# Optimization experiments

Hardware: AMD Instinct MI355X
Metric: run time of the kernel (lower is better)

Reference implementation:

```python
import jax, jax.numpy as jnp
import numpy as np

B, T, F, H = 64, 2048, 128, 32  # batch, seq_len, input_features, lstm hidden


def setup_inputs() -> dict:
    key = jax.random.key(0)
    ks = jax.random.split(key, 4)
    X = jax.random.normal(ks[0], (B, T, F), dtype=jnp.float32)
    # combined gate weights, order (i, f, g, o) as in flax.linen.LSTMCell
    Wx = jax.random.normal(ks[1], (F, 4 * H), dtype=jnp.float32) / np.float32(np.sqrt(F))
    Wh = jax.random.normal(ks[2], (H, 4 * H), dtype=jnp.float32) / np.float32(np.sqrt(H))
    b = jnp.zeros((4 * H,), dtype=jnp.float32)
    Wd = jax.random.normal(ks[3], (H, 1), dtype=jnp.float32) / np.float32(np.sqrt(H))
    bd = jnp.zeros((1,), dtype=jnp.float32)
    return {"X": X, "Wx": Wx, "Wh": Wh, "b": b, "Wd": Wd, "bd": bd}


def reference(X, Wx, Wh, b, Wd, bd):
    # Precompute input->gate projections for all timesteps in one GEMM.
    xg = jnp.einsum('btf,fg->btg', X, Wx) + b  # [B, T, 4H]

    def step(carry, xg_t):
        c, h = carry
        g = xg_t + h @ Wh  # [B, 4H]
        i, f, gc, o = jnp.split(g, 4, axis=-1)
        c = jax.nn.sigmoid(f) * c + jax.nn.sigmoid(i) * jnp.tanh(gc)
        h = jax.nn.sigmoid(o) * jnp.tanh(c)
        return (c, h), None

    zeros = jnp.zeros((X.shape[0], H), X.dtype)
    (c_T, h_T), _ = jax.lax.scan(step, (zeros, zeros), jnp.swapaxes(xg, 0, 1))
    # Dense(1) applied to outputs, then last timestep selected == Dense on h_T
    return h_T @ Wd + bd  # [B, 1]
```

## Files before the change

kernel.cpp:

```cpp
#include <hip/hip_runtime.h>
#include <math.h>

#define BB 64
#define TT 2048
#define FF 128
#define HH 32
#define GG 128

#define S1f (-1.4426950408889634f)
#define S2f (-2.8853900817779268f)

typedef _Float16 half2_t __attribute__((ext_vector_type(2)));

__device__ __forceinline__ unsigned h2u(half2_t v) {
    unsigned u; __builtin_memcpy(&u, &v, 4); return u;
}
__device__ __forceinline__ half2_t u2h(unsigned u) {
    half2_t v; __builtin_memcpy(&v, &u, 4); return v;
}
__device__ __forceinline__ half2_t pkrtz(float a, float b) {
    auto r = __builtin_amdgcn_cvt_pkrtz(a, b);
    half2_t v; __builtin_memcpy(&v, &r, 4); return v;
}
__device__ __forceinline__ float rcp_(float x) { return __builtin_amdgcn_rcpf(x); }
__device__ __forceinline__ float exp2_(float x) { return __builtin_amdgcn_exp2f(x); }

#define DPP_(x, ctrl) \
    ((unsigned)__builtin_amdgcn_mov_dpp((int)(x), (ctrl), 0xF, 0xF, true))
#define CTRL_XOR1 0xB1
#define CTRL_XOR2 0x4E
#define CTRL_ROR4 0x124
#define CTRL_ROR8 0x128
#define SWZ16_(x) ((unsigned)__builtin_amdgcn_ds_swizzle((int)(x), 0x401F))

__global__ __launch_bounds__(256) void xg_gemm(const float* __restrict__ X,
                                               const float* __restrict__ Wx,
                                               const float* __restrict__ bias,
                                               float* __restrict__ xgT) {
    __shared__ float XL[64 * 32];
    __shared__ float WL[32 * 128];
    const int tid = threadIdx.x;
    const int row0 = blockIdx.x * 64;
    const int j0 = (tid & 15) * 8;
    const int r0 = (tid >> 4) * 4;

    float acc[4][8];
#pragma unroll
    for (int r = 0; r < 4; ++r)
#pragma unroll
        for (int jj = 0; jj < 8; ++jj) acc[r][jj] = 0.f;

    for (int f0 = 0; f0 < FF; f0 += 32) {
        __syncthreads();
        {
            const float4* src = (const float4*)(Wx + f0 * GG);
            float4* dst = (float4*)WL;
            dst[tid]       = src[tid];
            dst[tid + 256] = src[tid + 256];
            dst[tid + 512] = src[tid + 512];
            dst[tid + 768] = src[tid + 768];
        }
        {
            int lin = tid * 4;
            int row = lin >> 5;
            int fi  = lin & 31;
            ((float4*)XL)[tid] =
                *(const float4*)(X + (size_t)(row0 + row) * FF + f0 + fi);
            lin = (tid + 256) * 4;
            row = lin >> 5;
            fi  = lin & 31;
            ((float4*)XL)[tid + 256] =
                *(const float4*)(X + (size_t)(row0 + row) * FF + f0 + fi);
        }
        __syncthreads();
#pragma unroll 4
        for (int fi = 0; fi < 32; ++fi) {
            float xv[4];
#pragma unroll
            for (int r = 0; r < 4; ++r) xv[r] = XL[(r0 + r) * 32 + fi];
            float4 w0 = *(float4*)&WL[fi * GG + j0];
            float4 w1 = *(float4*)&WL[fi * GG + j0 + 4];
            float w[8] = {w0.x, w0.y, w0.z, w0.w, w1.x, w1.y, w1.z, w1.w};
#pragma unroll
            for (int r = 0; r < 4; ++r)
#pragma unroll
                for (int jj = 0; jj < 8; ++jj)
                    acc[r][jj] = fmaf(xv[r], w[jj], acc[r][jj]);
        }
    }
    const int b  = row0 >> 11;
    const int t0 = (row0 & 2047) + r0;
    float bl[8];
#pragma unroll
    for (int jj = 0; jj < 8; ++jj) bl[jj] = bias[j0 + jj];
#pragma unroll
    for (int jj = 0; jj < 8; ++jj) {
        const int j = j0 + jj;
        const float sc = (j >= 64 && j < 96) ? S2f : S1f;
        float4 o;
        o.x = (acc[0][jj] + bl[jj]) * sc;
        o.y = (acc[1][jj] + bl[jj]) * sc;
        o.z = (acc[2][jj] + bl[jj]) * sc;
        o.w = (acc[3][jj] + bl[jj]) * sc;
        *(float4*)(xgT + ((size_t)b * GG + j) * TT + t0) = o;
    }
}

__global__ __launch_bounds__(64) void lstm_rec(const float* __restrict__ xgT,
                                               const float* __restrict__ Wh,
                                               const float* __restrict__ Wd,
                                               const float* __restrict__ bd,
                                               float* __restrict__ out) {
    const int l = threadIdx.x;
    const int m = l & 31;
    const bool lo = (l < HH);
    const int b = blockIdx.x;

    unsigned iv[16];
    iv[0] = (unsigned)m;
    iv[1] = SWZ16_(iv[0]);
    iv[2] = DPP_(iv[0], CTRL_XOR2);
    iv[3] = DPP_(iv[1], CTRL_XOR2);
#pragma unroll
    for (int r = 0; r < 4; ++r) iv[4 + r] = DPP_(iv[r], CTRL_ROR4);
#pragma unroll
    for (int r = 0; r < 8; ++r) iv[8 + r] = DPP_(iv[r], CTRL_ROR8);

    const float scx = S1f;
    const float scy = lo ? S2f : S1f;
    half2_t whx[16], why[16];
#pragma unroll
    for (int r = 0; r < 16; ++r) {
        const int p  = (int)(iv[r] & 31u);
        const int p2 = p ^ 1;
        whx[r] = pkrtz(Wh[p * GG + l] * scx,       Wh[p2 * GG + l] * scx);
        why[r] = pkrtz(Wh[p * GG + l + 64] * scy,  Wh[p2 * GG + l + 64] * scy);
    }

    const float A1 = lo ? 2.f : 1.f;
    const float B1 = lo ? -1.f : 0.f;

    float h = 0.f;
    float c = 0.f;

    const float* pX = xgT + ((size_t)b * GG + l) * TT;
    const float* pY = xgT + ((size_t)b * GG + l + 64) * TT;

    float4 curX = *(const float4*)(pX);
    float4 curY = *(const float4*)(pY);
    float4 nxtX = *(const float4*)(pX + 4);
    float4 nxtY = *(const float4*)(pY + 4);

    auto step = [&](float xi, float xy) __attribute__((always_inline)) {
        unsigned g[16];
        unsigned hn = DPP_(__float_as_uint(h), CTRL_XOR1);
        g[0] = h2u(pkrtz(h, __uint_as_float(hn)));
        g[1] = SWZ16_(g[0]);
        g[2] = DPP_(g[0], CTRL_XOR2);
        g[3] = DPP_(g[1], CTRL_XOR2);
#pragma unroll
        for (int r = 0; r < 4; ++r) g[4 + r] = DPP_(g[r], CTRL_ROR4);
#pragma unroll
        for (int r = 0; r < 8; ++r) g[8 + r] = DPP_(g[r], CTRL_ROR8);

        float ax[4] = {xi, 0.f, 0.f, 0.f};
        float ay[4] = {xy, 0.f, 0.f, 0.f};
#pragma unroll
        for (int r = 0; r < 16; ++r) {
            half2_t hp = u2h(g[r]);
            ax[r & 3] = __builtin_amdgcn_fdot2(hp, whx[r], ax[r & 3], false);
            ay[r & 3] = __builtin_amdgcn_fdot2(hp, why[r], ay[r & 3], false);
        }
        float a0 = (ax[0] + ax[1]) + (ax[2] + ax[3]);
        float a1 = (ay[0] + ay[1]) + (ay[2] + ay[3]);

        float act0 = rcp_(1.f + exp2_(a0));
        float act1 = fmaf(A1, rcp_(1.f + exp2_(a1)), B1);

        auto pq = __builtin_amdgcn_permlane32_swap(__float_as_uint(act0),
                                                   __float_as_uint(act1), false, false);
        auto uv = __builtin_amdgcn_permlane32_swap(__float_as_uint(act1),
                                                   __float_as_uint(act0), false, false);
        float p = __uint_as_float(pq[0]);
        float q = __uint_as_float(pq[1]);
        float u = __uint_as_float(uv[0]);
        float v = __uint_as_float(uv[1]);

        float f_all = lo ? q : act0;
        float o_all = lo ? v : act1;
        c = fmaf(f_all, c, u * p);
        float tc = fmaf(2.f, rcp_(1.f + exp2_(c * S2f)), -1.f);
        h = o_all * tc;
    };

#pragma unroll 1
    for (int t4 = 0; t4 < TT; t4 += 4) {
        float4 uX = curX, uY = curY;
        curX = nxtX; curY = nxtY;
        if (t4 + 8 < TT) {
            nxtX = *(const float4*)(pX + t4 + 8);
            nxtY = *(const float4*)(pY + t4 + 8);
        }
        step(uX.x, uY.x);
        step(uX.y, uY.y);
        step(uX.z, uY.z);
        step(uX.w, uY.w);
    }

    float contrib = h * Wd[m];
#pragma unroll
    for (int off = 32; off >= 1; off >>= 1)
        contrib += __shfl_xor(contrib, off, 64);
    if (l == 0) out[b] = fmaf(0.5f, contrib, bd[0]);
}

extern "C" void kernel_launch(void* const* d_in, const int* in_sizes, int n_in,
                              void* d_out, int out_size, void* d_ws, size_t ws_size,
                              hipStream_t stream) {
    const float* X    = (const float*)d_in[0];
    const float* Wx   = (const float*)d_in[1];
    const float* Wh   = (const float*)d_in[2];
    const float* bias = (const float*)d_in[3];
    const float* Wd   = (const float*)d_in[4];
    const float* bd   = (const float*)d_in[5];
    float* out = (float*)d_out;
    float* xgT = (float*)d_ws;

    hipLaunchKernelGGL(xg_gemm, dim3((BB * TT) / 64), dim3(256), 0, stream,
                       X, Wx, bias, xgT);
    hipLaunchKernelGGL(lstm_rec, dim3(BB), dim3(64), 0, stream,
                       xgT, Wh, Wd, bd, out);
}
```

Measured before the change: 509.5 us.

## Interleave four independent batch recurrences per wavefront to hide step latency

The recurrent kernel now has each 64-lane wavefront process four batch elements instead of one, stepping their independent LSTM chains in interleaved order so that one chain's dependent DPP, fdot2 and transcendental latency can overlap with another's. The grid shrinks from 64 to 16 blocks. The serial critical path per chain is unchanged, but per-step instruction work for a wave grows fourfold. It also uses more registers and fewer CUs, so it only pays off if the single-chain loop was latency-bound rather than issue-bound.

Measured after the change: 1.537 ms. +201.7%, slower.

```diff
diff --git a/kernel.cpp b/kernel.cpp
--- a/kernel.cpp
+++ b/kernel.cpp
@@ -6,6 +6,7 @@
 #define FF 128
 #define HH 32
 #define GG 128
+#define NC 4
 
 #define S1f (-1.4426950408889634f)
 #define S2f (-2.8853900817779268f)
@@ -114,7 +115,7 @@
     const int l = threadIdx.x;
     const int m = l & 31;
     const bool lo = (l < HH);
-    const int b = blockIdx.x;
+    const int b0 = blockIdx.x * NC;
 
     unsigned iv[16];
     iv[0] = (unsigned)m;
@@ -140,21 +141,26 @@
     const float A1 = lo ? 2.f : 1.f;
     const float B1 = lo ? -1.f : 0.f;
 
-    float h = 0.f;
-    float c = 0.f;
-
-    const float* pX = xgT + ((size_t)b * GG + l) * TT;
-    const float* pY = xgT + ((size_t)b * GG + l + 64) * TT;
-
-    float4 curX = *(const float4*)(pX);
-    float4 curY = *(const float4*)(pY);
-    float4 nxtX = *(const float4*)(pX + 4);
-    float4 nxtY = *(const float4*)(pY + 4);
-
-    auto step = [&](float xi, float xy) __attribute__((always_inline)) {
+    float h[NC], c[NC];
+    const float* pX[NC];
+    const float* pY[NC];
+    float4 curX[NC], curY[NC], nxtX[NC], nxtY[NC];
+#pragma unroll
+    for (int q = 0; q < NC; ++q) {
+        h[q] = 0.f; c[q] = 0.f;
+        pX[q] = xgT + ((size_t)(b0 + q) * GG + l) * TT;
+        pY[q] = xgT + ((size_t)(b0 + q) * GG + l + 64) * TT;
+        curX[q] = *(const float4*)(pX[q]);
+        curY[q] = *(const float4*)(pY[q]);
+        nxtX[q] = *(const float4*)(pX[q] + 4);
+        nxtY[q] = *(const float4*)(pY[q] + 4);
+    }
+
+    auto step = [&](float& hq, float& cq, float xi, float xy)
+        __attribute__((always_inline)) {
         unsigned g[16];
-        unsigned hn = DPP_(__float_as_uint(h), CTRL_XOR1);
-        g[0] = h2u(pkrtz(h, __uint_as_float(hn)));
+        unsigned hn = DPP_(__float_as_uint(hq), CTRL_XOR1);
+        g[0] = h2u(pkrtz(hq, __uint_as_float(hn)));
         g[1] = SWZ16_(g[0]);
         g[2] = DPP_(g[0], CTRL_XOR2);
         g[3] = DPP_(g[1], CTRL_XOR2);
@@ -188,30 +194,45 @@
 
         float f_all = lo ? q : act0;
         float o_all = lo ? v : act1;
-        c = fmaf(f_all, c, u * p);
-        float tc = fmaf(2.f, rcp_(1.f + exp2_(c * S2f)), -1.f);
-        h = o_all * tc;
+        cq = fmaf(f_all, cq, u * p);
+        float tc = fmaf(2.f, rcp_(1.f + exp2_(cq * S2f)), -1.f);
+        hq = o_all * tc;
     };
 
 #pragma unroll 1
     for (int t4 = 0; t4 < TT; t4 += 4) {
-        float4 uX = curX, uY = curY;
-        curX = nxtX; curY = nxtY;
+        float4 uX[NC], uY[NC];
+#pragma unroll
+        for (int q = 0; q < NC; ++q) {
+            uX[q] = curX[q]; uY[q] = curY[q];
+            curX[q] = nxtX[q]; curY[q] = nxtY[q];
+        }
         if (t4 + 8 < TT) {
-            nxtX = *(const float4*)(pX + t4 + 8);
-            nxtY = *(const float4*)(pY + t4 + 8);
-        }
-        step(uX.x, uY.x);
-        step(uX.y, uY.y);
-        step(uX.z, uY.z);
-        step(uX.w, uY.w);
-    }
-
-    float contrib = h * Wd[m];
-#pragma unroll
-    for (int off = 32; off >= 1; off >>= 1)
-        contrib += __shfl_xor(contrib, off, 64);
-    if (l == 0) out[b] = fmaf(0.5f, contrib, bd[0]);
+#pragma unroll
+            for (int q = 0; q < NC; ++q) {
+                nxtX[q] = *(const float4*)(pX[q] + t4 + 8);
+                nxtY[q] = *(const float4*)(pY[q] + t4 + 8);
+            }
+        }
+#pragma unroll
+        for (int q = 0; q < NC; ++q) step(h[q], c[q], uX[q].x, uY[q].x);
+#pragma unroll
+        for (int q = 0; q < NC; ++q) step(h[q], c[q], uX[q].y, uY[q].y);
+#pragma unroll
+        for (int q = 0; q < NC; ++q) step(h[q], c[q], uX[q].z, uY[q].z);
+#pragma unroll
+        for (int q = 0; q < NC; ++q) step(h[q], c[q], uX[q].w, uY[q].w);
+    }
+
+    const float wd = Wd[m];
+#pragma unroll
+    for (int q = 0; q < NC; ++q) {
+        float contrib = h[q] * wd;
+#pragma unroll
+        for (int off = 32; off >= 1; off >>= 1)
+            contrib += __shfl_xor(contrib, off, 64);
+        if (l == 0) out[b0 + q] = fmaf(0.5f, contrib, bd[0]);
+    }
 }
 
 extern "C" void kernel_launch(void* const* d_in, const int* in_sizes, int n_in,
@@ -228,6 +249,6 @@
 
     hipLaunchKernelGGL(xg_gemm, dim3((BB * TT) / 64), dim3(256), 0, stream,
                        X, Wx, bias, xgT);
-    hipLaunchKernelGGL(lstm_rec, dim3(BB), dim3(64), 0, stream,
+    hipLaunchKernelGGL(lstm_rec, dim3(BB / NC), dim3(64), 0, stream,
                        xgT, Wh, Wd, bd, out);
 }
```
